# Kernel tuning notes

Hardware: AMD Instinct MI355X
Metric: run time of the kernel (lower is better)

The kernel has to match this reference:

```python
import jax, jax.numpy as jnp
import numpy as np

D = 512; H = 8; DFF = 2048; S1 = 1024; S2 = 512; B = 8; EPS = 1e-5


def setup_inputs() -> dict:
    key = jax.random.key(0)
    ks = jax.random.split(key, 10)
    def w(k, shape):
        return jax.random.normal(k, shape, dtype=jnp.float32) * 0.02
    return {
        "rna_embed": jax.random.normal(ks[0], (S1, B, D), dtype=jnp.float32),
        "protein_embed": jax.random.normal(ks[1], (S2, B, D), dtype=jnp.float32),
        # self-attention params (torch MHA packed in_proj)
        "Wqkv_s": w(ks[2], (3 * D, D)), "bqkv_s": jnp.zeros((3 * D,), jnp.float32),
        "Wo_s": w(ks[3], (D, D)), "bo_s": jnp.zeros((D,), jnp.float32),
        # cross-attention params
        "Wqkv_c": w(ks[4], (3 * D, D)), "bqkv_c": jnp.zeros((3 * D,), jnp.float32),
        "Wo_c": w(ks[5], (D, D)), "bo_c": jnp.zeros((D,), jnp.float32),
        # FFN params
        "W1": w(ks[6], (DFF, D)), "b1": jnp.zeros((DFF,), jnp.float32),
        "W2": w(ks[7], (D, DFF)), "b2": jnp.zeros((D,), jnp.float32),
        # LayerNorm params: norm0_1, norm1_1, norm1_2, norm2
        "g0": jnp.ones((D,), jnp.float32), "be0": jnp.zeros((D,), jnp.float32),
        "g11": jnp.ones((D,), jnp.float32), "be11": jnp.zeros((D,), jnp.float32),
        "g12": jnp.ones((D,), jnp.float32), "be12": jnp.zeros((D,), jnp.float32),
        "g2": jnp.ones((D,), jnp.float32), "be2": jnp.zeros((D,), jnp.float32),
    }


def _layernorm(x, g, b):
    m = jnp.mean(x, axis=-1, keepdims=True)
    v = jnp.mean(jnp.square(x - m), axis=-1, keepdims=True)
    return (x - m) * jax.lax.rsqrt(v + EPS) * g + b


def _mha(xq, xkv, Wqkv, bqkv, Wo, bo):
    # xq: (Sq, B, D), xkv: (Sk, B, D)
    Wq, Wk, Wv = jnp.split(Wqkv, 3, axis=0)
    bq, bk, bv = jnp.split(bqkv, 3)
    hd = D // H
    scale = 1.0 / np.sqrt(hd).astype(np.float32)
    q = (xq @ Wq.T + bq).reshape(xq.shape[0], -1, H, hd)   # (Sq,B,H,hd)
    k = (xkv @ Wk.T + bk).reshape(xkv.shape[0], -1, H, hd)  # (Sk,B,H,hd)
    v = (xkv @ Wv.T + bv).reshape(xkv.shape[0], -1, H, hd)
    scores = jnp.einsum('qbhd,kbhd->bhqk', q, k) * scale    # (B,H,Sq,Sk)
    attn = jax.nn.softmax(scores, axis=-1)
    o = jnp.einsum('bhqk,kbhd->qbhd', attn, v).reshape(xq.shape[0], -1, D)
    return o @ Wo.T + bo


def reference(rna_embed, protein_embed, Wqkv_s, bqkv_s, Wo_s, bo_s,
              Wqkv_c, bqkv_c, Wo_c, bo_c, W1, b1, W2, b2,
              g0, be0, g11, be11, g12, be12, g2, be2):
    x1 = rna_embed
    # pre-norm self-attention
    h = _layernorm(x1, g0, be0)
    x1 = x1 + _mha(h, h, Wqkv_s, bqkv_s, Wo_s, bo_s)
    # pre-norm cross-attention (queries from x1, keys/values from protein)
    x1 = x1 + _mha(_layernorm(x1, g11, be11), _layernorm(protein_embed, g12, be12),
                   Wqkv_c, bqkv_c, Wo_c, bo_c)
    # pre-norm FFN
    h = _layernorm(x1, g2, be2)
    x1 = x1 + (jax.nn.relu(h @ W1.T + b1) @ W2.T + b2)
    return x1
```

## Files before the change

kernel.cpp:

```cpp
#include <hip/hip_runtime.h>

typedef unsigned short u16;
typedef unsigned int u32;
typedef u16 u16x8 __attribute__((ext_vector_type(8)));
typedef u16 u16x4 __attribute__((ext_vector_type(4)));
typedef short bfx8 __attribute__((ext_vector_type(8)));
typedef float f32x4 __attribute__((ext_vector_type(4)));

#define AS1 __attribute__((address_space(1)))
#define AS3 __attribute__((address_space(3)))

__device__ __forceinline__ u16 f2bf(float f) {
  union { float f; u32 u; } c; c.f = f;
  u32 u = c.u;
  u += 0x7fffu + ((u >> 16) & 1u);
  return (u16)(u >> 16);
}

__device__ __forceinline__ u32 cvt_pk_bf16(float lo, float hi) {
  u32 r;
  asm("v_cvt_pk_bf16_f32 %0, %1, %2" : "=v"(r) : "v"(lo), "v"(hi));
  return r;
}

__device__ __forceinline__ float fexp2(float x) {
  float r;
  asm("v_exp_f32 %0, %1" : "=v"(r) : "v"(x));
  return r;
}

__device__ __forceinline__ void ln_row(const float* __restrict__ x,
                                       const float* __restrict__ g,
                                       const float* __restrict__ be,
                                       u16* __restrict__ out, int gw, int lane) {
  const float4* row = (const float4*)(x + (size_t)gw * 512);
  float4 a = row[2 * lane], b = row[2 * lane + 1];
  float s = a.x + a.y + a.z + a.w + b.x + b.y + b.z + b.w;
  float q = a.x*a.x + a.y*a.y + a.z*a.z + a.w*a.w + b.x*b.x + b.y*b.y + b.z*b.z + b.w*b.w;
#pragma unroll
  for (int m = 1; m < 64; m <<= 1) { s += __shfl_xor(s, m); q += __shfl_xor(q, m); }
  float mean = s * (1.f / 512.f);
  float var = q * (1.f / 512.f) - mean * mean;
  float rs = rsqrtf(var + 1e-5f);
  const float4* g4 = (const float4*)g;
  const float4* b4 = (const float4*)be;
  float4 ga = g4[2 * lane], gb = g4[2 * lane + 1];
  float4 ba = b4[2 * lane], bb = b4[2 * lane + 1];
  u16x8 o;
  o[0] = f2bf((a.x - mean) * rs * ga.x + ba.x);
  o[1] = f2bf((a.y - mean) * rs * ga.y + ba.y);
  o[2] = f2bf((a.z - mean) * rs * ga.z + ba.z);
  o[3] = f2bf((a.w - mean) * rs * ga.w + ba.w);
  o[4] = f2bf((b.x - mean) * rs * gb.x + bb.x);
  o[5] = f2bf((b.y - mean) * rs * gb.y + bb.y);
  o[6] = f2bf((b.z - mean) * rs * gb.z + bb.z);
  o[7] = f2bf((b.w - mean) * rs * gb.w + bb.w);
  ((u16x8*)(out + (size_t)gw * 512))[lane] = o;
}

__global__ __launch_bounds__(256) void cvtln_kernel(const float* __restrict__ a0, const float* __restrict__ a1,
                                                    const float* __restrict__ a2, const float* __restrict__ a3,
                                                    const float* __restrict__ a4, const float* __restrict__ a5,
                                                    u16* __restrict__ b0, u16* __restrict__ b1,
                                                    u16* __restrict__ b2, u16* __restrict__ b3,
                                                    u16* __restrict__ b4, u16* __restrict__ b5,
                                                    const float* __restrict__ x, const float* __restrict__ g,
                                                    const float* __restrict__ be, u16* __restrict__ lnout) {
  if (blockIdx.x < 4096) {
    int i = blockIdx.x * 256 + threadIdx.x;
    const float* s; u16* d; int off;
    if      (i < 196608) { s = a0; d = b0; off = i; }
    else if (i < 262144) { s = a1; d = b1; off = i - 196608; }
    else if (i < 458752) { s = a2; d = b2; off = i - 262144; }
    else if (i < 524288) { s = a3; d = b3; off = i - 458752; }
    else if (i < 786432) { s = a4; d = b4; off = i - 524288; }
    else                 { s = a5; d = b5; off = i - 786432; }
    float4 v = ((const float4*)s)[off];
    u16x4 o;
    o[0] = f2bf(v.x); o[1] = f2bf(v.y); o[2] = f2bf(v.z); o[3] = f2bf(v.w);
    ((u16x4*)d)[off] = o;
  } else {
    int gw = ((blockIdx.x - 4096) * 256 + threadIdx.x) >> 6;
    ln_row(x, g, be, lnout, gw, threadIdx.x & 63);
  }
}

__global__ __launch_bounds__(256) void ln_kernel(const float* __restrict__ x,
                                                 const float* __restrict__ g,
                                                 const float* __restrict__ be,
                                                 u16* __restrict__ out, int ntok) {
  int gw = (blockIdx.x * 256 + threadIdx.x) >> 6;
  if (gw >= ntok) return;
  ln_row(x, g, be, out, gw, threadIdx.x & 63);
}

__global__ __launch_bounds__(256) void ln2_kernel(const float* __restrict__ xa, const float* __restrict__ ga,
                                                  const float* __restrict__ ba, u16* __restrict__ oa,
                                                  const float* __restrict__ xb, const float* __restrict__ gb,
                                                  const float* __restrict__ bb, u16* __restrict__ ob) {
  int lane = threadIdx.x & 63;
  if (blockIdx.x < 2048) {
    int gw = (blockIdx.x * 256 + threadIdx.x) >> 6;
    ln_row(xa, ga, ba, oa, gw, lane);
  } else {
    int gw = ((blockIdx.x - 2048) * 256 + threadIdx.x) >> 6;
    ln_row(xb, gb, bb, ob, gw, lane);
  }
}

__global__ __launch_bounds__(256) void vt_kernel(const u16* __restrict__ vB, u16* __restrict__ vt,
                                                 int stride, int S) {
  __shared__ u16 lt[64 * 68];
  const int t = threadIdx.x;
  const int b = blockIdx.y, h = blockIdx.z;
  const int sr = t >> 3, dc = (t & 7) * 8;
#pragma unroll
  for (int p = 0; p < 2; ++p) {
    int s = blockIdx.x * 64 + sr + p * 32;
    u16x8 v = *(const u16x8*)(vB + (size_t)(s * 8 + b) * stride + h * 64 + dc);
    u16x4 lo, hi;
    lo[0]=v[0]; lo[1]=v[1]; lo[2]=v[2]; lo[3]=v[3];
    hi[0]=v[4]; hi[1]=v[5]; hi[2]=v[6]; hi[3]=v[7];
    *(u16x4*)&lt[(sr + p * 32) * 68 + dc] = lo;
    *(u16x4*)&lt[(sr + p * 32) * 68 + dc + 4] = hi;
  }
  __syncthreads();
#pragma unroll
  for (int p = 0; p < 2; ++p) {
    int d = sr + p * 32;
    u16x8 o;
#pragma unroll
    for (int e = 0; e < 8; ++e) o[e] = lt[(dc + e) * 68 + d];
    *(u16x8*)(vt + ((size_t)(b * 8 + h) * 64 + d) * S + blockIdx.x * 64 + dc) = o;
  }
}

template <int EPI, int BM, int BN>
__device__ __forceinline__ void gemm8_body(const u16* __restrict__ A,
                                           const u16* __restrict__ Bw,
                                           const float* __restrict__ bias,
                                           const float* __restrict__ res,
                                           void* __restrict__ Cout,
                                           int M, int K, int bn, int bm) {
  constexpr int WCg = BN / 64;
  constexpr int WRg = 8 / WCg;
  constexpr int RPW = BM / WRg;
  constexpr int IM = RPW / 16;
  constexpr int LD = (BM + BN) / 64;
  __shared__ __align__(16) u16 lA[2][BM * 64];
  __shared__ __align__(16) u16 lB[2][BN * 64];
  const int tid = threadIdx.x;
  const int lane = tid & 63, w = tid >> 6;
  const int wr = w / WCg, wc = w % WCg;
  const int r15 = lane & 15, kg = lane >> 4;
  const int xr = (r15 & 7) << 4;

  f32x4 acc[IM][4] = {};

  const int lrw = tid >> 3;
  const int lcl = ((tid & 7) * 8) ^ ((lrw & 7) * 8);
  const u16* gA = A + (size_t)(bn + lrw) * K + lcl;
  const u16* gB = Bw + (size_t)(bm + lrw) * K + lcl;
  const int ldsbase = (w * 8) * 64;

#define STAGE8(buf, t) do {                                                               \
    _Pragma("unroll")                                                                     \
    for (int i_ = 0; i_ < BM / 64; ++i_)                                                  \
      __builtin_amdgcn_global_load_lds((AS1 u32*)(gA + (size_t)(i_ * 64) * K + (t) * 64), \
                                       (AS3 u32*)&lA[buf][i_ * 4096 + ldsbase], 16, 0, 0);\
    _Pragma("unroll")                                                                     \
    for (int i_ = 0; i_ < BN / 64; ++i_)                                                  \
      __builtin_amdgcn_global_load_lds((AS1 u32*)(gB + (size_t)(i_ * 64) * K + (t) * 64), \
                                       (AS3 u32*)&lB[buf][i_ * 4096 + ldsbase], 16, 0, 0);\
  } while (0)

  const int nk = K >> 6;
  STAGE8(0, 0);
  for (int t = 0; t < nk; ++t) {
    const int cur = t & 1;
    if (t + 1 < nk) {
      STAGE8(cur ^ 1, t + 1);
      if constexpr (LD == 3)      asm volatile("s_waitcnt vmcnt(3)" ::: "memory");
      else if constexpr (LD == 4) asm volatile("s_waitcnt vmcnt(4)" ::: "memory");
      else                        asm volatile("s_waitcnt vmcnt(8)" ::: "memory");
    } else {
      asm volatile("s_waitcnt vmcnt(0)" ::: "memory");
    }
    __builtin_amdgcn_sched_barrier(0);
    __builtin_amdgcn_s_barrier();
    __builtin_amdgcn_sched_barrier(0);

    const char* Ac = (const char*)lA[cur];
    const char* Bc = (const char*)lB[cur];
    __builtin_amdgcn_s_setprio(1);
#pragma unroll
    for (int kk = 0; kk < 2; ++kk) {
      bfx8 a[IM], b[4];
#pragma unroll
      for (int i = 0; i < IM; ++i)
        a[i] = *(const bfx8*)(Ac + (wr * RPW + i * 16 + r15) * 128 + ((kk * 64 + kg * 16) ^ xr));
#pragma unroll
      for (int j = 0; j < 4; ++j)
        b[j] = *(const bfx8*)(Bc + (wc * 64 + j * 16 + r15) * 128 + ((kk * 64 + kg * 16) ^ xr));
#pragma unroll
      for (int i = 0; i < IM; ++i)
#pragma unroll
        for (int j = 0; j < 4; ++j)
          acc[i][j] = __builtin_amdgcn_mfma_f32_16x16x32_bf16(a[i], b[j], acc[i][j], 0, 0, 0);
    }
    __builtin_amdgcn_s_setprio(0);
    __builtin_amdgcn_sched_barrier(0);
    __builtin_amdgcn_s_barrier();
  }
#undef STAGE8

#pragma unroll
  for (int i = 0; i < IM; ++i) {
#pragma unroll
    for (int j = 0; j < 4; ++j) {
      int col = bm + wc * 64 + j * 16 + r15;
      float bv = bias[col];
#pragma unroll
      for (int r = 0; r < 4; ++r) {
        int row = bn + wr * RPW + i * 16 + kg * 4 + r;
        float v = acc[i][j][r] + bv;
        if (EPI == 1) v = fmaxf(v, 0.f);
        if (EPI == 2) {
          ((float*)Cout)[(size_t)row * M + col] = res[(size_t)row * M + col] + v;
        } else {
          ((u16*)Cout)[(size_t)row * M + col] = f2bf(v);
        }
      }
    }
  }
}

template <int EPI, int BM, int BN, int MINW>
__global__ __launch_bounds__(512, MINW) void gemm8(const u16* __restrict__ A,
                                                   const u16* __restrict__ Bw,
                                                   const float* __restrict__ bias,
                                                   const float* __restrict__ res,
                                                   void* __restrict__ Cout,
                                                   int N, int M, int K) {
  const int nwg = gridDim.x * gridDim.y;
  const int id = blockIdx.y * gridDim.x + blockIdx.x;
  const int swz = (id & 7) * (nwg >> 3) + (id >> 3);
  const int bn = (swz / gridDim.x) * BM;
  const int bm = (swz % gridDim.x) * BN;
  gemm8_body<EPI, BM, BN>(A, Bw, bias, res, Cout, M, K, bn, bm);
}

__global__ __launch_bounds__(512, 6) void gemm8_dual(const u16* __restrict__ A0, const u16* __restrict__ W0,
                                                     const float* __restrict__ c0, u16* __restrict__ O0,
                                                     const u16* __restrict__ A1, const u16* __restrict__ W1,
                                                     const float* __restrict__ c1, u16* __restrict__ O1) {
  const int id = blockIdx.x;
  const u16 *A, *Bw; const float* bias; u16* C; int M, gx, lid;
  if (id < 512) { A = A0; Bw = W0; bias = c0; C = O0; M = 512;  gx = 4; lid = id; }
  else          { A = A1; Bw = W1; bias = c1; C = O1; M = 1024; gx = 8; lid = id - 512; }
  const int swz = (lid & 7) * 64 + (lid >> 3);
  const int bn = (swz / gx) * 64;
  const int bm = (swz % gx) * 128;
  gemm8_body<0, 64, 128>(A, Bw, bias, nullptr, C, M, 512, bn, bm);
}

__global__ __launch_bounds__(512, 4) void attn_kernel(const u16* __restrict__ qB,
                                                      const u16* __restrict__ kB,
                                                      const u16* __restrict__ vtB,
                                                      u16* __restrict__ oB,
                                                      int qStride, int kvStride, int Sk) {
  __shared__ __align__(16) u16 lK[4][64 * 64];
  __shared__ __align__(16) u16 lVt[4][64 * 64];
  __shared__ __align__(16) u16 lP[8][16 * 64];
  const int tid = threadIdx.x, lane = tid & 63, w = tid >> 6;
  const int sid = blockIdx.x;
  const int h = sid & 7, b = (sid >> 3) & 7, qt = sid >> 6;
  const int r15 = lane & 15, kg = lane >> 4;
  const int srow = lane >> 3;
  const int sxcol = ((lane & 7) * 8) ^ (srow * 8);

  const int qs = qt * 128 + w * 16 + r15;
  const u16* qrow = qB + (size_t)(qs * 8 + b) * qStride + h * 64;
  bfx8 qf0 = *(const bfx8*)(qrow + kg * 8);
  bfx8 qf1 = *(const bfx8*)(qrow + 32 + kg * 8);

  const u16* vbase = vtB + ((size_t)(b * 8 + h) * 64) * Sk;
  const u16* kp0 = kB + ((size_t)(w * 8 + srow) * 8 + b) * kvStride + h * 64 + sxcol;
  const size_t kAdv = (size_t)64 * 8 * kvStride;
  const u16* vp0 = vbase + (size_t)(w * 8 + srow) * Sk + sxcol;

#define STAGE(buf, tt) do {                                                           \
    __builtin_amdgcn_global_load_lds((AS1 u32*)(kp0 + (size_t)(tt) * kAdv),           \
                                     (AS3 u32*)&lK[buf][(w * 8) * 64], 16, 0, 0);     \
    __builtin_amdgcn_global_load_lds((AS1 u32*)(vp0 + (size_t)(tt) * 64),             \
                                     (AS3 u32*)&lVt[buf][(w * 8) * 64], 16, 0, 0);    \
  } while (0)

  const int nt = Sk / 64;
  const int np = nt >> 1;
  STAGE(0, 0); STAGE(1, 1);

  f32x4 oacc[4] = {};
  float mrow = -1e30f, lsum = 0.f;
  const float C2 = 0.125f * 1.44269504088896340736f;
  const int xr = (r15 & 7) << 4;
  char* myP = (char*)lP[w];

  for (int i = 0; i < np; ++i) {
    const int ba = (i & 1) * 2, bb = ba + 1;
    __builtin_amdgcn_sched_barrier(0);
    __builtin_amdgcn_s_barrier();
    __builtin_amdgcn_sched_barrier(0);
    if (i + 1 < np) {
      const int sb = ((i + 1) & 1) * 2;
      STAGE(sb, 2 * (i + 1)); STAGE(sb + 1, 2 * (i + 1) + 1);
      asm volatile("s_waitcnt vmcnt(4)" ::: "memory");
    } else {
      asm volatile("s_waitcnt vmcnt(0)" ::: "memory");
    }
    __builtin_amdgcn_sched_barrier(0);

    const char* Ka = (const char*)lK[ba];
    const char* Kb = (const char*)lK[bb];
    f32x4 sa[4] = {}, sb_[4] = {};
    __builtin_amdgcn_s_setprio(1);
#pragma unroll
    for (int j = 0; j < 4; ++j) {
      const char* kpa = Ka + (j * 16 + r15) * 128;
      bfx8 ka0 = *(const bfx8*)(kpa + ((kg * 16) ^ xr));
      bfx8 ka1 = *(const bfx8*)(kpa + ((64 + kg * 16) ^ xr));
      sa[j] = __builtin_amdgcn_mfma_f32_16x16x32_bf16(ka0, qf0, sa[j], 0, 0, 0);
      sa[j] = __builtin_amdgcn_mfma_f32_16x16x32_bf16(ka1, qf1, sa[j], 0, 0, 0);
    }
#pragma unroll
    for (int j = 0; j < 4; ++j) {
      const char* kpb = Kb + (j * 16 + r15) * 128;
      bfx8 kb0 = *(const bfx8*)(kpb + ((kg * 16) ^ xr));
      bfx8 kb1 = *(const bfx8*)(kpb + ((64 + kg * 16) ^ xr));
      sb_[j] = __builtin_amdgcn_mfma_f32_16x16x32_bf16(kb0, qf0, sb_[j], 0, 0, 0);
      sb_[j] = __builtin_amdgcn_mfma_f32_16x16x32_bf16(kb1, qf1, sb_[j], 0, 0, 0);
    }
    __builtin_amdgcn_s_setprio(0);

    float lm = fmaxf(fmaxf(fmaxf(sa[0][0], sa[0][1]), fmaxf(sa[0][2], sa[0][3])),
              fmaxf(fmaxf(fmaxf(sa[1][0], sa[1][1]), fmaxf(sa[1][2], sa[1][3])),
              fmaxf(fmaxf(fmaxf(sa[2][0], sa[2][1]), fmaxf(sa[2][2], sa[2][3])),
                    fmaxf(fmaxf(sa[3][0], sa[3][1]), fmaxf(sa[3][2], sa[3][3])))));
    float lmb = fmaxf(fmaxf(fmaxf(sb_[0][0], sb_[0][1]), fmaxf(sb_[0][2], sb_[0][3])),
               fmaxf(fmaxf(fmaxf(sb_[1][0], sb_[1][1]), fmaxf(sb_[1][2], sb_[1][3])),
               fmaxf(fmaxf(fmaxf(sb_[2][0], sb_[2][1]), fmaxf(sb_[2][2], sb_[2][3])),
                     fmaxf(fmaxf(sb_[3][0], sb_[3][1]), fmaxf(sb_[3][2], sb_[3][3])))));
    lm = fmaxf(lm, lmb);

    if (!__all(lm <= mrow + 16.0f)) {
      float m0 = fmaxf(lm, __shfl_xor(lm, 16));
      m0 = fmaxf(m0, __shfl_xor(m0, 32));
      float mn = fmaxf(mrow, m0);
      float corr = fexp2((mrow - mn) * C2);
      mrow = mn;
      lsum *= corr;
#pragma unroll
      for (int jd = 0; jd < 4; ++jd)
#pragma unroll
        for (int r = 0; r < 4; ++r) oacc[jd][r] *= corr;
    }
    float bc = -mrow * C2;

    float pa[4][4], pb[4][4];
#pragma unroll
    for (int j = 0; j < 4; ++j)
#pragma unroll
      for (int r = 0; r < 4; ++r) {
        pa[j][r] = fexp2(fmaf(sa[j][r], C2, bc));
        pb[j][r] = fexp2(fmaf(sb_[j][r], C2, bc));
      }
    float ps = 0.f;
#pragma unroll
    for (int j = 0; j < 4; ++j)
#pragma unroll
      for (int r = 0; r < 4; ++r) ps += pa[j][r] + pb[j][r];
    lsum += ps;

#pragma unroll
    for (int j = 0; j < 4; ++j)
#pragma unroll
      for (int h2 = 0; h2 < 2; ++h2) {
        u32 pk = cvt_pk_bf16(pa[j][2 * h2], pa[j][2 * h2 + 1]);
        int k0b = (j * 16 + kg * 4 + 2 * h2) * 2;
        *(u32*)(myP + r15 * 128 + (k0b ^ xr)) = pk;
      }
    const char* Va = (const char*)lVt[ba];
    __builtin_amdgcn_s_setprio(1);
#pragma unroll
    for (int s2 = 0; s2 < 2; ++s2) {
      bfx8 ptf = *(const bfx8*)(myP + r15 * 128 + ((s2 * 64 + kg * 16) ^ xr));
#pragma unroll
      for (int jd = 0; jd < 4; ++jd) {
        const char* vp = Va + (jd * 16 + r15) * 128;
        bfx8 vf = *(const bfx8*)(vp + ((s2 * 64 + kg * 16) ^ xr));
        oacc[jd] = __builtin_amdgcn_mfma_f32_16x16x32_bf16(vf, ptf, oacc[jd], 0, 0, 0);
      }
    }
    __builtin_amdgcn_s_setprio(0);

#pragma unroll
    for (int j = 0; j < 4; ++j)
#pragma unroll
      for (int h2 = 0; h2 < 2; ++h2) {
        u32 pk = cvt_pk_bf16(pb[j][2 * h2], pb[j][2 * h2 + 1]);
        int k0b = (j * 16 + kg * 4 + 2 * h2) * 2;
        *(u32*)(myP + r15 * 128 + (k0b ^ xr)) = pk;
      }
    const char* Vb = (const char*)lVt[bb];
    __builtin_amdgcn_s_setprio(1);
#pragma unroll
    for (int s2 = 0; s2 < 2; ++s2) {
      bfx8 ptf = *(const bfx8*)(myP + r15 * 128 + ((s2 * 64 + kg * 16) ^ xr));
#pragma unroll
      for (int jd = 0; jd < 4; ++jd) {
        const char* vp = Vb + (jd * 16 + r15) * 128;
        bfx8 vf = *(const bfx8*)(vp + ((s2 * 64 + kg * 16) ^ xr));
        oacc[jd] = __builtin_amdgcn_mfma_f32_16x16x32_bf16(vf, ptf, oacc[jd], 0, 0, 0);
      }
    }
    __builtin_amdgcn_s_setprio(0);
  }
#undef STAGE

  lsum += __shfl_xor(lsum, 16);
  lsum += __shfl_xor(lsum, 32);
  float inv = 1.f / lsum;
  const int s = qt * 128 + w * 16 + r15;
  u16* orow = oB + (size_t)(s * 8 + b) * 512 + h * 64;
#pragma unroll
  for (int jd = 0; jd < 4; ++jd) {
    u32 p0 = cvt_pk_bf16(oacc[jd][0] * inv, oacc[jd][1] * inv);
    u32 p1 = cvt_pk_bf16(oacc[jd][2] * inv, oacc[jd][3] * inv);
    *(u32*)(orow + jd * 16 + kg * 4) = p0;
    *(u32*)(orow + jd * 16 + kg * 4 + 2) = p1;
  }
}

extern "C" void kernel_launch(void* const* d_in, const int* in_sizes, int n_in,
                              void* d_out, int out_size, void* d_ws, size_t ws_size,
                              hipStream_t stream) {
  const float* rna    = (const float*)d_in[0];
  const float* prot   = (const float*)d_in[1];
  const float* Wqkv_s = (const float*)d_in[2];
  const float* bqkv_s = (const float*)d_in[3];
  const float* Wo_s   = (const float*)d_in[4];
  const float* bo_s   = (const float*)d_in[5];
  const float* Wqkv_c = (const float*)d_in[6];
  const float* bqkv_c = (const float*)d_in[7];
  const float* Wo_c   = (const float*)d_in[8];
  const float* bo_c   = (const float*)d_in[9];
  const float* W1     = (const float*)d_in[10];
  const float* b1     = (const float*)d_in[11];
  const float* W2     = (const float*)d_in[12];
  const float* b2     = (const float*)d_in[13];
  const float* g0  = (const float*)d_in[14];
  const float* be0 = (const float*)d_in[15];
  const float* g11 = (const float*)d_in[16];
  const float* be11= (const float*)d_in[17];
  const float* g12 = (const float*)d_in[18];
  const float* be12= (const float*)d_in[19];
  const float* g2  = (const float*)d_in[20];
  const float* be2 = (const float*)d_in[21];
  float* out = (float*)d_out;

  u16* wbf      = (u16*)d_ws;
  u16* w_qkv_s  = wbf;
  u16* w_o_s    = wbf + 786432;
  u16* w_qkv_c  = wbf + 1048576;
  u16* w_o_c    = wbf + 1835008;
  u16* w_1      = wbf + 2097152;
  u16* w_2      = wbf + 3145728;
  u16* hbuf     = wbf + 4194304;
  u16* qkv      = hbuf + 4194304;
  u16* kvc      = qkv + 4194304;
  u16* attnO    = qkv + 12582912;
  u16* hp       = attnO + 4194304;
  u16* ffnmid   = qkv;

  cvtln_kernel<<<6144, 256, 0, stream>>>(Wqkv_s, Wo_s, Wqkv_c, Wo_c, W1, W2,
                                         w_qkv_s, w_o_s, w_qkv_c, w_o_c, w_1, w_2,
                                         rna, g0, be0, hbuf);

  gemm8<0, 256, 256, 2><<<dim3(6, 32), 512, 0, stream>>>(hbuf, w_qkv_s, bqkv_s, nullptr, qkv, 8192, 1536, 512);
  vt_kernel<<<dim3(16, 8, 8), 256, 0, stream>>>(qkv + 1024, hbuf, 1536, 1024);
  attn_kernel<<<512, 512, 0, stream>>>(qkv, qkv + 512, hbuf, attnO, 1536, 1536, 1024);
  gemm8<2, 64, 128, 6><<<dim3(4, 128), 512, 0, stream>>>(attnO, w_o_s, bo_s, rna, out, 8192, 512, 512);

  ln2_kernel<<<3072, 256, 0, stream>>>(out, g11, be11, hbuf, prot, g12, be12, hp);
  gemm8_dual<<<1024, 512, 0, stream>>>(hbuf, w_qkv_c, bqkv_c, qkv,
                                       hp, w_qkv_c + 512 * 512, bqkv_c + 512, kvc);
  vt_kernel<<<dim3(8, 8, 8), 256, 0, stream>>>(kvc + 512, hp, 1024, 512);
  attn_kernel<<<512, 512, 0, stream>>>(qkv, kvc, hp, attnO, 512, 1024, 512);
  gemm8<2, 64, 128, 6><<<dim3(4, 128), 512, 0, stream>>>(attnO, w_o_c, bo_c, out, out, 8192, 512, 512);

  ln_kernel<<<2048, 256, 0, stream>>>(out, g2, be2, hbuf, 8192);
  gemm8<1, 256, 256, 2><<<dim3(8, 32), 512, 0, stream>>>(hbuf, w_1, b1, nullptr, ffnmid, 8192, 2048, 512);
  gemm8<2, 64, 128, 6><<<dim3(4, 128), 512, 0, stream>>>(ffnmid, w_2, b2, out, out, 8192, 512, 2048);
}
```

Baseline: 201.5 us.

## Store intermediate residual stream in bf16 and retile QKV GEMM to 128x128

The residual stream between sublayers (after self-attention and after cross-attention) is now stored as bf16 instead of fp32. New GEMM epilogues write and read bf16 residuals, and the LayerNorm kernels read bf16 input. This halves the traffic for the intermediate residual reads and writes. Separately, the self-attention QKV projection GEMM moves from 256x256 to 128x128 tiles with a larger grid and higher occupancy. The trade-off is lost precision in the residual path, since rounding errors accumulate across sublayers.

New measurement: 191.5 us. -5.0%, faster.

```diff
diff --git a/kernel.cpp b/kernel.cpp
--- a/kernel.cpp
+++ b/kernel.cpp
@@ -17,6 +17,11 @@
   return (u16)(u >> 16);
 }
 
+__device__ __forceinline__ float bf2f(u16 b) {
+  union { u32 u; float f; } c; c.u = ((u32)b) << 16;
+  return c.f;
+}
+
 __device__ __forceinline__ u32 cvt_pk_bf16(float lo, float hi) {
   u32 r;
   asm("v_cvt_pk_bf16_f32 %0, %1, %2" : "=v"(r) : "v"(lo), "v"(hi));
@@ -29,14 +34,12 @@
   return r;
 }
 
-__device__ __forceinline__ void ln_row(const float* __restrict__ x,
-                                       const float* __restrict__ g,
-                                       const float* __restrict__ be,
-                                       u16* __restrict__ out, int gw, int lane) {
-  const float4* row = (const float4*)(x + (size_t)gw * 512);
-  float4 a = row[2 * lane], b = row[2 * lane + 1];
-  float s = a.x + a.y + a.z + a.w + b.x + b.y + b.z + b.w;
-  float q = a.x*a.x + a.y*a.y + a.z*a.z + a.w*a.w + b.x*b.x + b.y*b.y + b.z*b.z + b.w*b.w;
+__device__ __forceinline__ void ln_core(float f[8], const float* __restrict__ g,
+                                        const float* __restrict__ be,
+                                        u16* __restrict__ out, int gw, int lane) {
+  float s = 0.f, q = 0.f;
+#pragma unroll
+  for (int e = 0; e < 8; ++e) { s += f[e]; q += f[e] * f[e]; }
 #pragma unroll
   for (int m = 1; m < 64; m <<= 1) { s += __shfl_xor(s, m); q += __shfl_xor(q, m); }
   float mean = s * (1.f / 512.f);
@@ -46,16 +49,31 @@
   const float4* b4 = (const float4*)be;
   float4 ga = g4[2 * lane], gb = g4[2 * lane + 1];
   float4 ba = b4[2 * lane], bb = b4[2 * lane + 1];
+  float gv[8] = {ga.x, ga.y, ga.z, ga.w, gb.x, gb.y, gb.z, gb.w};
+  float bv[8] = {ba.x, ba.y, ba.z, ba.w, bb.x, bb.y, bb.z, bb.w};
   u16x8 o;
-  o[0] = f2bf((a.x - mean) * rs * ga.x + ba.x);
-  o[1] = f2bf((a.y - mean) * rs * ga.y + ba.y);
-  o[2] = f2bf((a.z - mean) * rs * ga.z + ba.z);
-  o[3] = f2bf((a.w - mean) * rs * ga.w + ba.w);
-  o[4] = f2bf((b.x - mean) * rs * gb.x + bb.x);
-  o[5] = f2bf((b.y - mean) * rs * gb.y + bb.y);
-  o[6] = f2bf((b.z - mean) * rs * gb.z + bb.z);
-  o[7] = f2bf((b.w - mean) * rs * gb.w + bb.w);
+#pragma unroll
+  for (int e = 0; e < 8; ++e) o[e] = f2bf((f[e] - mean) * rs * gv[e] + bv[e]);
   ((u16x8*)(out + (size_t)gw * 512))[lane] = o;
+}
+
+__device__ __forceinline__ void ln_row_f32(const float* __restrict__ x, const float* __restrict__ g,
+                                           const float* __restrict__ be, u16* __restrict__ out,
+                                           int gw, int lane) {
+  const float4* row = (const float4*)(x + (size_t)gw * 512);
+  float4 a = row[2 * lane], b = row[2 * lane + 1];
+  float f[8] = {a.x, a.y, a.z, a.w, b.x, b.y, b.z, b.w};
+  ln_core(f, g, be, out, gw, lane);
+}
+
+__device__ __forceinline__ void ln_row_bf16(const u16* __restrict__ x, const float* __restrict__ g,
+                                            const float* __restrict__ be, u16* __restrict__ out,
+                                            int gw, int lane) {
+  u16x8 v = ((const u16x8*)(x + (size_t)gw * 512))[lane];
+  float f[8];
+#pragma unroll
+  for (int e = 0; e < 8; ++e) f[e] = bf2f(v[e]);
+  ln_core(f, g, be, out, gw, lane);
 }
 
 __global__ __launch_bounds__(256) void cvtln_kernel(const float* __restrict__ a0, const float* __restrict__ a1,
@@ -81,30 +99,30 @@
     ((u16x4*)d)[off] = o;
   } else {
     int gw = ((blockIdx.x - 4096) * 256 + threadIdx.x) >> 6;
-    ln_row(x, g, be, lnout, gw, threadIdx.x & 63);
-  }
-}
-
-__global__ __launch_bounds__(256) void ln_kernel(const float* __restrict__ x,
-                                                 const float* __restrict__ g,
-                                                 const float* __restrict__ be,
-                                                 u16* __restrict__ out, int ntok) {
+    ln_row_f32(x, g, be, lnout, gw, threadIdx.x & 63);
+  }
+}
+
+__global__ __launch_bounds__(256) void lnb_kernel(const u16* __restrict__ x,
+                                                  const float* __restrict__ g,
+                                                  const float* __restrict__ be,
+                                                  u16* __restrict__ out, int ntok) {
   int gw = (blockIdx.x * 256 + threadIdx.x) >> 6;
   if (gw >= ntok) return;
-  ln_row(x, g, be, out, gw, threadIdx.x & 63);
-}
-
-__global__ __launch_bounds__(256) void ln2_kernel(const float* __restrict__ xa, const float* __restrict__ ga,
+  ln_row_bf16(x, g, be, out, gw, threadIdx.x & 63);
+}
+
+__global__ __launch_bounds__(256) void ln2_kernel(const u16* __restrict__ xa, const float* __restrict__ ga,
                                                   const float* __restrict__ ba, u16* __restrict__ oa,
                                                   const float* __restrict__ xb, const float* __restrict__ gb,
                                                   const float* __restrict__ bb, u16* __restrict__ ob) {
   int lane = threadIdx.x & 63;
   if (blockIdx.x < 2048) {
     int gw = (blockIdx.x * 256 + threadIdx.x) >> 6;
-    ln_row(xa, ga, ba, oa, gw, lane);
+    ln_row_bf16(xa, ga, ba, oa, gw, lane);
   } else {
     int gw = ((blockIdx.x - 2048) * 256 + threadIdx.x) >> 6;
-    ln_row(xb, gb, bb, ob, gw, lane);
+    ln_row_f32(xb, gb, bb, ob, gw, lane);
   }
 }
 
@@ -139,7 +157,7 @@
 __device__ __forceinline__ void gemm8_body(const u16* __restrict__ A,
                                            const u16* __restrict__ Bw,
                                            const float* __restrict__ bias,
-                                           const float* __restrict__ res,
+                                           const void* __restrict__ res,
                                            void* __restrict__ Cout,
                                            int M, int K, int bn, int bm) {
   constexpr int WCg = BN / 64;
@@ -223,12 +241,17 @@
 #pragma unroll
       for (int r = 0; r < 4; ++r) {
         int row = bn + wr * RPW + i * 16 + kg * 4 + r;
+        size_t idx = (size_t)row * M + col;
         float v = acc[i][j][r] + bv;
         if (EPI == 1) v = fmaxf(v, 0.f);
-        if (EPI == 2) {
-          ((float*)Cout)[(size_t)row * M + col] = res[(size_t)row * M + col] + v;
+        if (EPI == 3) {
+          ((u16*)Cout)[idx] = f2bf(((const float*)res)[idx] + v);
+        } else if (EPI == 4) {
+          ((u16*)Cout)[idx] = f2bf(bf2f(((const u16*)res)[idx]) + v);
+        } else if (EPI == 5) {
+          ((float*)Cout)[idx] = bf2f(((const u16*)res)[idx]) + v;
         } else {
-          ((u16*)Cout)[(size_t)row * M + col] = f2bf(v);
+          ((u16*)Cout)[idx] = f2bf(v);
         }
       }
     }
@@ -239,7 +262,7 @@
 __global__ __launch_bounds__(512, MINW) void gemm8(const u16* __restrict__ A,
                                                    const u16* __restrict__ Bw,
                                                    const float* __restrict__ bias,
-                                                   const float* __restrict__ res,
+                                                   const void* __restrict__ res,
                                                    void* __restrict__ Cout,
                                                    int N, int M, int K) {
   const int nwg = gridDim.x * gridDim.y;
@@ -480,25 +503,27 @@
   u16* kvc      = qkv + 4194304;
   u16* attnO    = qkv + 12582912;
   u16* hp       = attnO + 4194304;
+  u16* x1b      = hp + 2097152;
+  u16* x1c      = x1b + 4194304;
   u16* ffnmid   = qkv;
 
   cvtln_kernel<<<6144, 256, 0, stream>>>(Wqkv_s, Wo_s, Wqkv_c, Wo_c, W1, W2,
                                          w_qkv_s, w_o_s, w_qkv_c, w_o_c, w_1, w_2,
                                          rna, g0, be0, hbuf);
 
-  gemm8<0, 256, 256, 2><<<dim3(6, 32), 512, 0, stream>>>(hbuf, w_qkv_s, bqkv_s, nullptr, qkv, 8192, 1536, 512);
+  gemm8<0, 128, 128, 4><<<dim3(12, 64), 512, 0, stream>>>(hbuf, w_qkv_s, bqkv_s, nullptr, qkv, 8192, 1536, 512);
   vt_kernel<<<dim3(16, 8, 8), 256, 0, stream>>>(qkv + 1024, hbuf, 1536, 1024);
   attn_kernel<<<512, 512, 0, stream>>>(qkv, qkv + 512, hbuf, attnO, 1536, 1536, 1024);
-  gemm8<2, 64, 128, 6><<<dim3(4, 128), 512, 0, stream>>>(attnO, w_o_s, bo_s, rna, out, 8192, 512, 512);
-
-  ln2_kernel<<<3072, 256, 0, stream>>>(out, g11, be11, hbuf, prot, g12, be12, hp);
+  gemm8<3, 64, 128, 6><<<dim3(4, 128), 512, 0, stream>>>(attnO, w_o_s, bo_s, rna, x1b, 8192, 512, 512);
+
+  ln2_kernel<<<3072, 256, 0, stream>>>(x1b, g11, be11, hbuf, prot, g12, be12, hp);
   gemm8_dual<<<1024, 512, 0, stream>>>(hbuf, w_qkv_c, bqkv_c, qkv,
                                        hp, w_qkv_c + 512 * 512, bqkv_c + 512, kvc);
   vt_kernel<<<dim3(8, 8, 8), 256, 0, stream>>>(kvc + 512, hp, 1024, 512);
   attn_kernel<<<512, 512, 0, stream>>>(qkv, kvc, hp, attnO, 512, 1024, 512);
-  gemm8<2, 64, 128, 6><<<dim3(4, 128), 512, 0, stream>>>(attnO, w_o_c, bo_c, out, out, 8192, 512, 512);
-
-  ln_kernel<<<2048, 256, 0, stream>>>(out, g2, be2, hbuf, 8192);
+  gemm8<4, 64, 128, 6><<<dim3(4, 128), 512, 0, stream>>>(attnO, w_o_c, bo_c, x1b, x1c, 8192, 512, 512);
+
+  lnb_kernel<<<2048, 256, 0, stream>>>(x1c, g2, be2, hbuf, 8192);
   gemm8<1, 256, 256, 2><<<dim3(8, 32), 512, 0, stream>>>(hbuf, w_1, b1, nullptr, ffnmid, 8192, 2048, 512);
-  gemm8<2, 64, 128, 6><<<dim3(4, 128), 512, 0, stream>>>(ffnmid, w_2, b2, out, out, 8192, 512, 2048);
-}
+  gemm8<5, 64, 128, 6><<<dim3(4, 128), 512, 0, stream>>>(ffnmid, w_2, b2, x1c, out, 8192, 512, 2048);
+}
```
